# Kernel optimization log

Hardware: AMD Instinct MI355X
Metric: run time of the kernel (lower is better)

Reference implementation:

```python
import jax, jax.numpy as jnp
import numpy as np

DIM = 5120
NUM_HEADS = 40
HEAD_DIM = DIM // NUM_HEADS
EPS = 1e-6


def rms_norm(x, g):
    # RMSNorm over last dim in fp32 for stability
    xf = x.astype(jnp.float32)
    inv = jax.lax.rsqrt(jnp.mean(xf * xf, axis=-1, keepdims=True) + EPS)
    return (xf * inv).astype(x.dtype) * g


def setup_inputs() -> dict:
    key = jax.random.key(0)
    ks = jax.random.split(key, 12)
    B, S, L = 1, 4096, 512
    inp = {
        "hidden_cond": jax.random.normal(ks[0], (B, S, DIM), jnp.float32),
        "hidden_uncond": jax.random.normal(ks[1], (B, S, DIM), jnp.float32),
        "context_cond": jax.random.normal(ks[2], (B, L, DIM), jnp.float32),
        "context_uncond": jax.random.normal(ks[3], (B, L, DIM), jnp.float32),
        # parameters (torch nn.Linear: y = x @ W.T + b)
        "Wq": jax.random.normal(ks[4], (DIM, DIM), jnp.float32) * (DIM ** -0.5),
        "bq": jnp.zeros((DIM,), jnp.float32),
        "Wkv": jax.random.normal(ks[5], (2 * DIM, DIM), jnp.float32) * (DIM ** -0.5),
        "bkv": jnp.zeros((2 * DIM,), jnp.float32),
        "gq": jnp.ones((DIM,), jnp.float32),
        "gk": jnp.ones((DIM,), jnp.float32),
        "Wo": jax.random.normal(ks[6], (DIM, DIM), jnp.float32) * (DIM ** -0.5),
        "bo": jnp.zeros((DIM,), jnp.float32),
    }
    return inp


def reference(hidden_cond, hidden_uncond, context_cond, context_uncond,
              Wq, bq, Wkv, bkv, gq, gk, Wo, bo):
    H, Dh = NUM_HEADS, HEAD_DIM
    scale = Dh ** -0.5

    hidden = jnp.concatenate([hidden_cond, hidden_uncond], axis=0)   # [2B, S, D]
    context = jnp.concatenate([context_cond, context_uncond], axis=0)  # [2B, L, D]
    CB, S, D = hidden.shape
    L = context.shape[1]

    q = hidden @ Wq.T + bq                    # [2B, S, D]
    q = rms_norm(q, gq)
    q = q.reshape(CB, S, H, Dh).transpose(0, 2, 1, 3)  # [2B, H, S, Dh]

    kv = context @ Wkv.T + bkv                # [2B, L, 2D]
    kv = kv.reshape(CB, L, 2, H, Dh).transpose(2, 0, 3, 1, 4)  # [2,2B,H,L,Dh]
    k, v = kv[0], kv[1]

    k_flat = k.transpose(0, 2, 1, 3).reshape(CB, L, D)
    k_flat = rms_norm(k_flat, gk)
    k = k_flat.reshape(CB, L, H, Dh).transpose(0, 2, 1, 3)  # [2B, H, L, Dh]

    attn = jnp.einsum('bhsd,bhld->bhsl', q, k) * scale
    attn = jax.nn.softmax(attn.astype(jnp.float32), axis=-1).astype(q.dtype)
    out = jnp.einsum('bhsl,bhld->bhsd', attn, v)            # [2B, H, S, Dh]
    out = out.transpose(0, 2, 1, 3).reshape(CB, S, D)
    out = out @ Wo.T + bo

    out_cond, out_uncond = jnp.split(out, 2, axis=0)
    return (out_cond, out_uncond)
```

## Files before the change

### kernel.cpp

```cpp
#include <hip/hip_runtime.h>
#include <hip/hip_bf16.h>
#include <cstdint>
#include <cstddef>

#define DIM 5120
#define NH 40
#define HD 128
#define S_LEN 4096
#define L_LEN 512
#define CBATCH 2
#define MQ (CBATCH*S_LEN)
#define ML (CBATCH*L_LEN)

typedef unsigned short ushort_t;
typedef __bf16 bf16x8 __attribute__((ext_vector_type(8)));
typedef float f32x4 __attribute__((ext_vector_type(4)));
typedef float f32x16 __attribute__((ext_vector_type(16)));

__device__ __forceinline__ ushort_t f2bf(float f) {
  union { float f; unsigned u; } c; c.f = f;
  unsigned r = c.u + 0x7fffu + ((c.u >> 16) & 1u);
  return (ushort_t)(r >> 16);
}

__device__ __forceinline__ void load_lds16(const void* g, void* l) {
  __builtin_amdgcn_global_load_lds(
      (const __attribute__((address_space(1))) void*)g,
      (__attribute__((address_space(3))) void*)l, 16, 0, 0);
}

__global__ __launch_bounds__(256) void cvt_f32_bf16(const float* __restrict__ in,
                                                    ushort_t* __restrict__ out, int n4) {
  int i = blockIdx.x * 256 + threadIdx.x;
  if (i >= n4) return;
  float4 v = *(const float4*)(in + 4ull * (size_t)i);
  ushort4 o;
  o.x = f2bf(v.x); o.y = f2bf(v.y); o.z = f2bf(v.z); o.w = f2bf(v.w);
  *(ushort4*)(out + 4ull * (size_t)i) = o;
}

template <int OUT_F32>
__global__ __launch_bounds__(512, 2) void gemm_bt8(const ushort_t* __restrict__ A,
                                                   const ushort_t* __restrict__ W,
                                                   const float* __restrict__ bias,
                                                   void* __restrict__ Cout,
                                                   int M, int N, int K) {
  __shared__ ushort_t lds[73728];
  char* ldsc = (char*)lds;
  const int tid = threadIdx.x;
  const int lane = tid & 63, w = tid >> 6;
  const int g = lane >> 4, c = lane & 15;
  const int wm = w >> 2, wn = w & 3;
  const int ntn = N >> 8;
  const int nwg = gridDim.x;
  int bid = blockIdx.x;
  bid = (bid & 7) * (nwg >> 3) + (bid >> 3);
  const int tm = bid / ntn, tn = bid % ntn;
  const size_t m0 = (size_t)tm * 256, n0 = (size_t)tn * 256;
  const ushort_t* Ab = A + m0 * (size_t)K;
  const ushort_t* Bb = W + n0 * (size_t)K;
  const int NT = K >> 6;

  const int srow = tid >> 2;
  const int sgq  = (tid & 3) ^ (((tid >> 5) & 1) << 1);
  const size_t rb0 = (size_t)srow * K + (size_t)sgq * 8;
  const size_t rb1 = rb0 + (size_t)128 * K;
  const int d0 = tid * 16;

  int offA[8], offB[4];
#pragma unroll
  for (int m = 0; m < 8; ++m) {
    int row = wm * 128 + m * 16 + c;
    offA[m] = row * 64 + ((g * 16) ^ ((row & 8) << 2));
  }
#pragma unroll
  for (int n = 0; n < 4; ++n) {
    int row = wn * 64 + n * 16 + c;
    offB[n] = row * 64 + ((g * 16) ^ ((row & 8) << 2));
  }

  auto STAGE = [&](int tIdx, int j, int dOff) {
    const size_t kof = (size_t)tIdx * 64 + (size_t)((j >> 1) << 5);
    const ushort_t* gsrc = ((j & 1) ? Ab : Bb) + kof;
    char* db = ldsc + dOff;
    load_lds16(gsrc + rb0, db + d0);
    load_lds16(gsrc + rb1, db + 8192 + d0);
  };
  auto nx = [](int x) { return (x + 16384 == 147456) ? 0 : x + 16384; };

  f32x4 acc[8][4] = {};

#pragma unroll
  for (int h = 0; h < 8; ++h) STAGE(h >> 2, h & 3, h * 16384);
  asm volatile("s_waitcnt vmcnt(8)" ::: "memory");
  __builtin_amdgcn_s_barrier();

  int rd = 0;
  int sOff = 131072;
  for (int t = 0; t < NT; ++t) {
    const int r0 = rd, r1 = nx(r0), r2 = nx(r1), r3 = nx(r2);
    bf16x8 a[4], a2[4], b[4];
#pragma unroll
    for (int m = 0; m < 4; ++m) a[m] = *(const bf16x8*)(ldsc + r1 + offA[m]);
#pragma unroll
    for (int n = 0; n < 4; ++n) b[n] = *(const bf16x8*)(ldsc + r0 + offB[n]);
    if (t < NT - 2) { STAGE(t + 2, 0, sOff); sOff = nx(sOff); }
    __builtin_amdgcn_s_barrier();
    asm volatile("s_waitcnt lgkmcnt(0)" ::: "memory");
    __builtin_amdgcn_sched_barrier(0);
    __builtin_amdgcn_s_setprio(1);
#pragma unroll
    for (int m = 0; m < 4; ++m)
#pragma unroll
      for (int n = 0; n < 4; ++n)
        acc[m][n] = __builtin_amdgcn_mfma_f32_16x16x32_bf16(a[m], b[n], acc[m][n], 0, 0, 0);
    __builtin_amdgcn_s_setprio(0);
    __builtin_amdgcn_s_barrier();
#pragma unroll
    for (int m = 0; m < 4; ++m) a2[m] = *(const bf16x8*)(ldsc + r1 + offA[4 + m]);
    if (t < NT - 2) { STAGE(t + 2, 1, sOff); sOff = nx(sOff); }
    __builtin_amdgcn_s_barrier();
    asm volatile("s_waitcnt lgkmcnt(0)" ::: "memory");
    __builtin_amdgcn_sched_barrier(0);
    __builtin_amdgcn_s_setprio(1);
#pragma unroll
    for (int m = 0; m < 4; ++m)
#pragma unroll
      for (int n = 0; n < 4; ++n)
        acc[4 + m][n] = __builtin_amdgcn_mfma_f32_16x16x32_bf16(a2[m], b[n], acc[4 + m][n], 0, 0, 0);
    __builtin_amdgcn_s_setprio(0);
    __builtin_amdgcn_s_barrier();
#pragma unroll
    for (int m = 0; m < 4; ++m) a[m] = *(const bf16x8*)(ldsc + r3 + offA[m]);
#pragma unroll
    for (int n = 0; n < 4; ++n) b[n] = *(const bf16x8*)(ldsc + r2 + offB[n]);
    if (t < NT - 2) { STAGE(t + 2, 2, sOff); sOff = nx(sOff); }
    __builtin_amdgcn_s_barrier();
    asm volatile("s_waitcnt lgkmcnt(0)" ::: "memory");
    __builtin_amdgcn_sched_barrier(0);
    __builtin_amdgcn_s_setprio(1);
#pragma unroll
    for (int m = 0; m < 4; ++m)
#pragma unroll
      for (int n = 0; n < 4; ++n)
        acc[m][n] = __builtin_amdgcn_mfma_f32_16x16x32_bf16(a[m], b[n], acc[m][n], 0, 0, 0);
    __builtin_amdgcn_s_setprio(0);
    __builtin_amdgcn_s_barrier();
#pragma unroll
    for (int m = 0; m < 4; ++m) a2[m] = *(const bf16x8*)(ldsc + r3 + offA[4 + m]);
    if (t < NT - 2) { STAGE(t + 2, 3, sOff); sOff = nx(sOff); }
    __builtin_amdgcn_s_barrier();
    asm volatile("s_waitcnt lgkmcnt(0)" ::: "memory");
    __builtin_amdgcn_sched_barrier(0);
    __builtin_amdgcn_s_setprio(1);
#pragma unroll
    for (int m = 0; m < 4; ++m)
#pragma unroll
      for (int n = 0; n < 4; ++n)
        acc[4 + m][n] = __builtin_amdgcn_mfma_f32_16x16x32_bf16(a2[m], b[n], acc[4 + m][n], 0, 0, 0);
    __builtin_amdgcn_s_setprio(0);
    if (t < NT - 2)       asm volatile("s_waitcnt vmcnt(6)" ::: "memory");
    else if (t == NT - 2) asm volatile("s_waitcnt vmcnt(0)" ::: "memory");
    __builtin_amdgcn_s_barrier();
    rd = nx(r3);
  }

#pragma unroll
  for (int m = 0; m < 8; ++m) {
#pragma unroll
    for (int n = 0; n < 4; ++n) {
      size_t gm = m0 + wm * 128 + m * 16 + g * 4;
      size_t gn = n0 + wn * 64 + n * 16 + c;
      float bn = bias[gn];
#pragma unroll
      for (int r = 0; r < 4; ++r) {
        float v = acc[m][n][r] + bn;
        if (OUT_F32) ((float*)Cout)[(gm + r) * (size_t)N + gn] = v;
        else         ((ushort_t*)Cout)[(gm + r) * (size_t)N + gn] = f2bf(v);
      }
    }
  }
  (void)M;
}

template <int OUT_F32>
__global__ __launch_bounds__(256) void gemm_bt(const ushort_t* __restrict__ A,
                                               const ushort_t* __restrict__ W,
                                               const float* __restrict__ bias,
                                               void* __restrict__ Cout,
                                               int M, int N, int K) {
  __shared__ ushort_t sA[128 * 32];
  __shared__ ushort_t sB[128 * 32];
  const int tid = threadIdx.x;
  const int w = tid >> 6, lane = tid & 63;
  const int g = lane >> 4, c = lane & 15;
  const int ntn = N >> 7;
  const int nwg = gridDim.x;
  int bid = blockIdx.x;
  bid = (bid & 7) * (nwg >> 3) + (bid >> 3);
  const int tm = bid / ntn, tn = bid % ntn;
  const size_t m0 = (size_t)tm * 128, n0 = (size_t)tn * 128;
  const int wr = (w >> 1) * 64, wc = (w & 1) * 64;

  f32x4 acc[4][4] = {};

  const ushort_t* Abase = A + m0 * (size_t)K;
  const ushort_t* Bbase = W + n0 * (size_t)K;

  for (int k0 = 0; k0 < K; k0 += 32) {
    __syncthreads();
#pragma unroll
    for (int i = 0; i < 2; ++i) {
      int gid = i * 256 + tid;
      int row = gid >> 2, colE = (gid & 3) << 3;
      load_lds16(Abase + (size_t)row * K + k0 + colE, sA + i * 2048 + w * 512);
      load_lds16(Bbase + (size_t)row * K + k0 + colE, sB + i * 2048 + w * 512);
    }
    __syncthreads();
    bf16x8 a[4], b[4];
#pragma unroll
    for (int m = 0; m < 4; ++m)
      a[m] = *(const bf16x8*)(sA + (wr + m * 16 + c) * 32 + g * 8);
#pragma unroll
    for (int n = 0; n < 4; ++n)
      b[n] = *(const bf16x8*)(sB + (wc + n * 16 + c) * 32 + g * 8);
#pragma unroll
    for (int m = 0; m < 4; ++m)
#pragma unroll
      for (int n = 0; n < 4; ++n)
        acc[m][n] = __builtin_amdgcn_mfma_f32_16x16x32_bf16(a[m], b[n], acc[m][n], 0, 0, 0);
  }

#pragma unroll
  for (int m = 0; m < 4; ++m) {
#pragma unroll
    for (int n = 0; n < 4; ++n) {
      size_t gm = m0 + wr + m * 16 + g * 4;
      size_t gn = n0 + wc + n * 16 + c;
      float bn = bias[gn];
#pragma unroll
      for (int r = 0; r < 4; ++r) {
        float v = acc[m][n][r] + bn;
        if (OUT_F32) ((float*)Cout)[(gm + r) * (size_t)N + gn] = v;
        else         ((ushort_t*)Cout)[(gm + r) * (size_t)N + gn] = f2bf(v);
      }
    }
  }
}

__global__ __launch_bounds__(256) void rmsnorm_rows(ushort_t* __restrict__ x,
                                                    const float* __restrict__ gw,
                                                    int ncols, int stride, float oscale) {
  const int row = blockIdx.x;
  ushort_t* p = x + (size_t)row * stride;
  const int tid = threadIdx.x;
  const int nch = ncols >> 3;
  float ss = 0.f;
  for (int ci = tid; ci < nch; ci += 256) {
    bf16x8 v = *(const bf16x8*)(p + ci * 8);
#pragma unroll
    for (int j = 0; j < 8; ++j) { float f = (float)v[j]; ss += f * f; }
  }
#pragma unroll
  for (int off = 1; off < 64; off <<= 1) ss += __shfl_xor(ss, off);
  __shared__ float sred[4];
  if ((tid & 63) == 0) sred[tid >> 6] = ss;
  __syncthreads();
  float tot = sred[0] + sred[1] + sred[2] + sred[3];
  float inv = rsqrtf(tot / (float)ncols + 1e-6f) * oscale;
  for (int ci = tid; ci < nch; ci += 256) {
    bf16x8 v = *(const bf16x8*)(p + ci * 8);
    bf16x8 ov;
#pragma unroll
    for (int j = 0; j < 8; ++j) {
      float f = (float)v[j];
      ushort_t ob = f2bf(f * inv * gw[ci * 8 + j]);
      ov[j] = *(__bf16*)&ob;
    }
    *(bf16x8*)(p + ci * 8) = ov;
  }
}

__global__ __launch_bounds__(256) void transpose_v(const ushort_t* __restrict__ kv,
                                                   ushort_t* __restrict__ vt) {
  const int bh = blockIdx.y, b = bh / NH, h = bh % NH;
  const int l0 = blockIdx.x * 32;
  const ushort_t* src = kv + (size_t)b * L_LEN * (2 * DIM) + DIM + (size_t)h * HD;
  ushort_t* dst = vt + (size_t)bh * HD * L_LEN;
  __shared__ ushort_t tile[32][HD + 16];
  const int tid = threadIdx.x;
#pragma unroll
  for (int i = 0; i < 2; ++i) {
    int gid = i * 256 + tid;
    int r = gid >> 4, ce = (gid & 15) << 3;
    *(bf16x8*)(&tile[r][ce]) = *(const bf16x8*)(src + (size_t)(l0 + r) * (2 * DIM) + ce);
  }
  __syncthreads();
#pragma unroll
  for (int i = 0; i < 2; ++i) {
    int gid = i * 256 + tid;
    int d = gid >> 2, le = (gid & 3) << 3;
    bf16x8 v;
#pragma unroll
    for (int j = 0; j < 8; ++j) v[j] = *(__bf16*)&tile[le + j][d];
    *(bf16x8*)(dst + (size_t)d * L_LEN + l0 + le) = v;
  }
}

__global__ __launch_bounds__(256) void attn_fwd(const ushort_t* __restrict__ q,
                                                const ushort_t* __restrict__ kv,
                                                const ushort_t* __restrict__ vt,
                                                ushort_t* __restrict__ out) {
  const int bh = blockIdx.y, b = bh / NH, h = bh % NH;
  const int tid = threadIdx.x, w = tid >> 6, lane = tid & 63;
  const int lq = lane & 31, hi = lane >> 5;
  const int qr0 = blockIdx.x * 128 + w * 32;

  __shared__ ushort_t sK[2][4096];
  __shared__ ushort_t sV[2][4096];

  const int skl = tid >> 3, skc = tid & 7;
  const ushort_t* kgsrc = kv + ((size_t)b * L_LEN + skl) * (2 * DIM)
                             + (size_t)h * HD + skc * 16;
  ushort_t* kd0 = &sK[0][(skc * 2) * 256 + skl * 8];
  ushort_t* kd1 = &sK[0][(skc * 2 + 1) * 256 + skl * 8];
  const int svd = tid >> 1, svh = tid & 1;
  const ushort_t* vgsrc = vt + (size_t)bh * HD * L_LEN + (size_t)svd * L_LEN + svh * 16;
  ushort_t* vd0 = &sV[0][(svh * 2) * 1024 + svd * 8];
  ushort_t* vd1 = &sV[0][(svh * 2 + 1) * 1024 + svd * 8];

  const ushort_t* qrow = q + ((size_t)b * S_LEN + qr0 + lq) * DIM + (size_t)h * HD + hi * 8;
  bf16x8 qf[8];
#pragma unroll
  for (int ks = 0; ks < 8; ++ks) qf[ks] = *(const bf16x8*)(qrow + ks * 16);

  f32x16 o[4];
#pragma unroll
  for (int ch = 0; ch < 4; ++ch) o[ch] = 0.f;
  float m = -1e30f, lsum = 0.f;

  {
    uint4 ka = *(const uint4*)kgsrc;
    uint4 kb = *(const uint4*)(kgsrc + 8);
    uint4 va = *(const uint4*)vgsrc;
    uint4 vb = *(const uint4*)(vgsrc + 8);
    *(uint4*)kd0 = ka; *(uint4*)kd1 = kb;
    *(uint4*)vd0 = va; *(uint4*)vd1 = vb;
  }
  __syncthreads();

  const int NT = L_LEN / 32;
  int buf = 0;
  for (int t = 0; t < NT; ++t) {
    uint4 ka, kb, va, vb;
    if (t + 1 < NT) {
      const ushort_t* kg = kgsrc + (size_t)(t + 1) * 32 * (2 * DIM);
      const ushort_t* vg = vgsrc + (t + 1) * 32;
      ka = *(const uint4*)kg; kb = *(const uint4*)(kg + 8);
      va = *(const uint4*)vg; vb = *(const uint4*)(vg + 8);
    }

    const ushort_t* kbuf = sK[buf];
    const ushort_t* vbuf = sV[buf];

    f32x16 sv = 0.f;
#pragma unroll
    for (int ks = 0; ks < 8; ++ks) {
      bf16x8 kf = *(const bf16x8*)(kbuf + (ks * 2 + hi) * 256 + lq * 8);
      sv = __builtin_amdgcn_mfma_f32_32x32x16_bf16(kf, qf[ks], sv, 0, 0, 0);
    }
    float pm = fmaxf(fmaxf(fmaxf(sv[0], sv[1]), fmaxf(sv[2], sv[3])),
                     fmaxf(fmaxf(sv[4], sv[5]), fmaxf(sv[6], sv[7])));
    pm = fmaxf(pm, fmaxf(fmaxf(fmaxf(sv[8], sv[9]), fmaxf(sv[10], sv[11])),
                         fmaxf(fmaxf(sv[12], sv[13]), fmaxf(sv[14], sv[15]))));
    pm = fmaxf(pm, __shfl_xor(pm, 32));
    if (__ballot(pm > m + 8.0f)) {
      float mn = fmaxf(m, pm);
      float al = __builtin_amdgcn_exp2f(m - mn);
      lsum *= al;
      m = mn;
#pragma unroll
      for (int r = 0; r < 16; ++r) {
        float ar = __shfl(al, (r & 3) + 8 * (r >> 2) + 4 * hi);
        o[0][r] *= ar; o[1][r] *= ar; o[2][r] *= ar; o[3][r] *= ar;
      }
    }
    float p[16]; float ls = 0.f;
#pragma unroll
    for (int r = 0; r < 16; ++r) { p[r] = __builtin_amdgcn_exp2f(sv[r] - m); ls += p[r]; }
    ls += __shfl_xor(ls, 32);
    lsum += ls;
    bf16x8 pa[2];
#pragma unroll
    for (int ks = 0; ks < 2; ++ks) {
      unsigned w0 = (unsigned)f2bf(p[8 * ks + 0]) | ((unsigned)f2bf(p[8 * ks + 1]) << 16);
      unsigned w1 = (unsigned)f2bf(p[8 * ks + 2]) | ((unsigned)f2bf(p[8 * ks + 3]) << 16);
      unsigned w2 = (unsigned)f2bf(p[8 * ks + 4]) | ((unsigned)f2bf(p[8 * ks + 5]) << 16);
      unsigned w3 = (unsigned)f2bf(p[8 * ks + 6]) | ((unsigned)f2bf(p[8 * ks + 7]) << 16);
      unsigned e0 = __shfl_xor((int)w0, 32), e1 = __shfl_xor((int)w1, 32);
      unsigned e2 = __shfl_xor((int)w2, 32), e3 = __shfl_xor((int)w3, 32);
      unsigned d0 = hi ? e2 : w0, d1 = hi ? e3 : w1;
      unsigned d2 = hi ? w2 : e0, d3 = hi ? w3 : e1;
      unsigned tmp[4] = {d0, d1, d2, d3};
      pa[ks] = *(const bf16x8*)tmp;
    }
#pragma unroll
    for (int ch = 0; ch < 4; ++ch) {
#pragma unroll
      for (int ks = 0; ks < 2; ++ks) {
        bf16x8 vf = *(const bf16x8*)(vbuf + (ks * 2 + hi) * 1024 + (ch * 32 + lq) * 8);
        o[ch] = __builtin_amdgcn_mfma_f32_32x32x16_bf16(pa[ks], vf, o[ch], 0, 0, 0);
      }
    }

    if (t + 1 < NT) {
      const int nb = buf ^ 1;
      *(uint4*)(kd0 + nb * 4096) = ka; *(uint4*)(kd1 + nb * 4096) = kb;
      *(uint4*)(vd0 + nb * 4096) = va; *(uint4*)(vd1 + nb * 4096) = vb;
    }
    __syncthreads();
    buf ^= 1;
  }

  float inv[16];
#pragma unroll
  for (int r = 0; r < 16; ++r) {
    float lr = __shfl(lsum, (r & 3) + 8 * (r >> 2) + 4 * hi);
    inv[r] = 1.0f / lr;
  }
  ushort_t* ob = out + ((size_t)b * S_LEN + qr0) * DIM + (size_t)h * HD;
#pragma unroll
  for (int ch = 0; ch < 4; ++ch)
#pragma unroll
    for (int r = 0; r < 16; ++r) {
      int row = (r & 3) + 8 * (r >> 2) + 4 * hi;
      ob[(size_t)row * DIM + ch * 32 + lq] = f2bf(o[ch][r] * inv[r]);
    }
}

extern "C" void kernel_launch(void* const* d_in, const int* in_sizes, int n_in,
                              void* d_out, int out_size, void* d_ws, size_t ws_size,
                              hipStream_t stream) {
  (void)in_sizes; (void)n_in; (void)out_size; (void)ws_size;
  const float* hidden_c = (const float*)d_in[0];
  const float* hidden_u = (const float*)d_in[1];
  const float* ctx_c    = (const float*)d_in[2];
  const float* ctx_u    = (const float*)d_in[3];
  const float* Wq  = (const float*)d_in[4];
  const float* bq  = (const float*)d_in[5];
  const float* Wkv = (const float*)d_in[6];
  const float* bkv = (const float*)d_in[7];
  const float* gq  = (const float*)d_in[8];
  const float* gk  = (const float*)d_in[9];
  const float* Wo  = (const float*)d_in[10];
  const float* bo  = (const float*)d_in[11];

  char* ws = (char*)d_ws;
  size_t off = 0;
  auto alloc = [&](size_t bytes) {
    char* p = ws + off; off += (bytes + 255) & ~(size_t)255; return p;
  };
  ushort_t* hbf  = (ushort_t*)alloc((size_t)MQ * DIM * 2);
  ushort_t* cbf  = (ushort_t*)alloc((size_t)ML * DIM * 2);
  ushort_t* wqb  = (ushort_t*)alloc((size_t)DIM * DIM * 2);
  ushort_t* wkvb = (ushort_t*)alloc((size_t)2 * DIM * DIM * 2);
  ushort_t* kvb  = (ushort_t*)alloc((size_t)ML * 2 * DIM * 2);
  ushort_t* vtb  = (ushort_t*)alloc((size_t)CBATCH * NH * HD * L_LEN * 2);
  ushort_t* qb   = (ushort_t*)d_out;

  auto cvt = [&](const float* in, ushort_t* o, size_t n) {
    int n4 = (int)(n >> 2);
    cvt_f32_bf16<<<dim3((n4 + 255) / 256), dim3(256), 0, stream>>>(in, o, n4);
  };
  cvt(hidden_c, hbf, (size_t)S_LEN * DIM);
  cvt(hidden_u, hbf + (size_t)S_LEN * DIM, (size_t)S_LEN * DIM);
  cvt(ctx_c, cbf, (size_t)L_LEN * DIM);
  cvt(ctx_u, cbf + (size_t)L_LEN * DIM, (size_t)L_LEN * DIM);
  cvt(Wq, wqb, (size_t)DIM * DIM);
  cvt(Wkv, wkvb, (size_t)2 * DIM * DIM);

  gemm_bt8<0><<<dim3((MQ / 256) * (DIM / 256)), dim3(512), 0, stream>>>(
      hbf, wqb, bq, (void*)qb, MQ, DIM, DIM);
  gemm_bt<0><<<dim3((ML / 128) * ((2 * DIM) / 128)), dim3(256), 0, stream>>>(
      cbf, wkvb, bkv, (void*)kvb, ML, 2 * DIM, DIM);
  cvt(Wo, wqb, (size_t)DIM * DIM);

  const float qscale = 0.08838834764831845f * 1.4426950408889634f;
  rmsnorm_rows<<<dim3(MQ), dim3(256), 0, stream>>>(qb, gq, DIM, DIM, qscale);
  rmsnorm_rows<<<dim3(ML), dim3(256), 0, stream>>>(kvb, gk, DIM, 2 * DIM, 1.0f);
  transpose_v<<<dim3(L_LEN / 32, CBATCH * NH), dim3(256), 0, stream>>>(kvb, vtb);

  attn_fwd<<<dim3(S_LEN / 128, CBATCH * NH), dim3(256), 0, stream>>>(qb, kvb, vtb, hbf);

  gemm_bt8<1><<<dim3((MQ / 256) * (DIM / 256)), dim3(512), 0, stream>>>(
      hbf, wqb, bo, d_out, MQ, DIM, DIM);
}
```

Baseline: 1.432 ms.

## Fuse Q and KV projection GEMMs into one launch using the 256x256 core

Extracts the 256x256 MFMA GEMM body into a shared device function and launches the Q projection and KV projection as one 800-block grid, with blocks 0-639 doing Q and the rest doing KV. The KV projection moves from the simpler 128x128 tile kernel to the larger pipelined tile. K is made a compile-time constant. The intent is to remove the weak KV GEMM and fill the tail of the Q GEMM wave with KV work, at the cost of hard-coded grid sizes and block swizzling across the mixed grid.

```diff
diff --git a/kernel.cpp b/kernel.cpp
--- a/kernel.cpp
+++ b/kernel.cpp
@@ -40,26 +40,18 @@
 }
 
 template <int OUT_F32>
-__global__ __launch_bounds__(512, 2) void gemm_bt8(const ushort_t* __restrict__ A,
-                                                   const ushort_t* __restrict__ W,
-                                                   const float* __restrict__ bias,
-                                                   void* __restrict__ Cout,
-                                                   int M, int N, int K) {
-  __shared__ ushort_t lds[73728];
-  char* ldsc = (char*)lds;
+__device__ __forceinline__ void gemm_core(const ushort_t* __restrict__ Ab,
+                                          const ushort_t* __restrict__ Bb,
+                                          const float* __restrict__ bias,
+                                          void* __restrict__ Cout,
+                                          int N, size_t m0, size_t n0,
+                                          char* ldsc) {
   const int tid = threadIdx.x;
   const int lane = tid & 63, w = tid >> 6;
   const int g = lane >> 4, c = lane & 15;
   const int wm = w >> 2, wn = w & 3;
-  const int ntn = N >> 8;
-  const int nwg = gridDim.x;
-  int bid = blockIdx.x;
-  bid = (bid & 7) * (nwg >> 3) + (bid >> 3);
-  const int tm = bid / ntn, tn = bid % ntn;
-  const size_t m0 = (size_t)tm * 256, n0 = (size_t)tn * 256;
-  const ushort_t* Ab = A + m0 * (size_t)K;
-  const ushort_t* Bb = W + n0 * (size_t)K;
-  const int NT = K >> 6;
+  constexpr int K = DIM;
+  constexpr int NT = K >> 6;
 
   const int srow = tid >> 2;
   const int sgq  = (tid & 3) ^ (((tid >> 5) & 1) << 1);
@@ -180,72 +172,41 @@
       }
     }
   }
-  (void)M;
-}
-
-template <int OUT_F32>
-__global__ __launch_bounds__(256) void gemm_bt(const ushort_t* __restrict__ A,
-                                               const ushort_t* __restrict__ W,
-                                               const float* __restrict__ bias,
-                                               void* __restrict__ Cout,
-                                               int M, int N, int K) {
-  __shared__ ushort_t sA[128 * 32];
-  __shared__ ushort_t sB[128 * 32];
-  const int tid = threadIdx.x;
-  const int w = tid >> 6, lane = tid & 63;
-  const int g = lane >> 4, c = lane & 15;
-  const int ntn = N >> 7;
-  const int nwg = gridDim.x;
+}
+
+__global__ __launch_bounds__(512, 2) void gemm_fused_qkv(
+    const ushort_t* __restrict__ hbf, const ushort_t* __restrict__ wq,
+    const ushort_t* __restrict__ cbf, const ushort_t* __restrict__ wkv,
+    const float* __restrict__ bq, const float* __restrict__ bkv,
+    ushort_t* __restrict__ qb, ushort_t* __restrict__ kvb) {
+  __shared__ ushort_t lds[73728];
+  char* ldsc = (char*)lds;
+  const int nwg = 800;
   int bid = blockIdx.x;
   bid = (bid & 7) * (nwg >> 3) + (bid >> 3);
-  const int tm = bid / ntn, tn = bid % ntn;
-  const size_t m0 = (size_t)tm * 128, n0 = (size_t)tn * 128;
-  const int wr = (w >> 1) * 64, wc = (w & 1) * 64;
-
-  f32x4 acc[4][4] = {};
-
-  const ushort_t* Abase = A + m0 * (size_t)K;
-  const ushort_t* Bbase = W + n0 * (size_t)K;
-
-  for (int k0 = 0; k0 < K; k0 += 32) {
-    __syncthreads();
-#pragma unroll
-    for (int i = 0; i < 2; ++i) {
-      int gid = i * 256 + tid;
-      int row = gid >> 2, colE = (gid & 3) << 3;
-      load_lds16(Abase + (size_t)row * K + k0 + colE, sA + i * 2048 + w * 512);
-      load_lds16(Bbase + (size_t)row * K + k0 + colE, sB + i * 2048 + w * 512);
-    }
-    __syncthreads();
-    bf16x8 a[4], b[4];
-#pragma unroll
-    for (int m = 0; m < 4; ++m)
-      a[m] = *(const bf16x8*)(sA + (wr + m * 16 + c) * 32 + g * 8);
-#pragma unroll
-    for (int n = 0; n < 4; ++n)
-      b[n] = *(const bf16x8*)(sB + (wc + n * 16 + c) * 32 + g * 8);
-#pragma unroll
-    for (int m = 0; m < 4; ++m)
-#pragma unroll
-      for (int n = 0; n < 4; ++n)
-        acc[m][n] = __builtin_amdgcn_mfma_f32_16x16x32_bf16(a[m], b[n], acc[m][n], 0, 0, 0);
-  }
-
-#pragma unroll
-  for (int m = 0; m < 4; ++m) {
-#pragma unroll
-    for (int n = 0; n < 4; ++n) {
-      size_t gm = m0 + wr + m * 16 + g * 4;
-      size_t gn = n0 + wc + n * 16 + c;
-      float bn = bias[gn];
-#pragma unroll
-      for (int r = 0; r < 4; ++r) {
-        float v = acc[m][n][r] + bn;
-        if (OUT_F32) ((float*)Cout)[(gm + r) * (size_t)N + gn] = v;
-        else         ((ushort_t*)Cout)[(gm + r) * (size_t)N + gn] = f2bf(v);
-      }
-    }
-  }
+  if (bid < 640) {
+    const int tm = bid / 20, tn = bid % 20;
+    const size_t m0 = (size_t)tm * 256, n0 = (size_t)tn * 256;
+    gemm_core<0>(hbf + m0 * DIM, wq + n0 * DIM, bq, qb, DIM, m0, n0, ldsc);
+  } else {
+    const int e = bid - 640;
+    const int tm = e / 40, tn = e % 40;
+    const size_t m0 = (size_t)tm * 256, n0 = (size_t)tn * 256;
+    gemm_core<0>(cbf + m0 * DIM, wkv + n0 * DIM, bkv, kvb, 2 * DIM, m0, n0, ldsc);
+  }
+}
+
+__global__ __launch_bounds__(512, 2) void gemm_out(
+    const ushort_t* __restrict__ A, const ushort_t* __restrict__ W,
+    const float* __restrict__ bias, float* __restrict__ C) {
+  __shared__ ushort_t lds[73728];
+  char* ldsc = (char*)lds;
+  const int nwg = 640;
+  int bid = blockIdx.x;
+  bid = (bid & 7) * (nwg >> 3) + (bid >> 3);
+  const int tm = bid / 20, tn = bid % 20;
+  const size_t m0 = (size_t)tm * 256, n0 = (size_t)tn * 256;
+  gemm_core<1>(A + m0 * DIM, W + n0 * DIM, bias, C, DIM, m0, n0, ldsc);
 }
 
 __global__ __launch_bounds__(256) void rmsnorm_rows(ushort_t* __restrict__ x,
@@ -479,10 +440,8 @@
   cvt(Wq, wqb, (size_t)DIM * DIM);
   cvt(Wkv, wkvb, (size_t)2 * DIM * DIM);
 
-  gemm_bt8<0><<<dim3((MQ / 256) * (DIM / 256)), dim3(512), 0, stream>>>(
-      hbf, wqb, bq, (void*)qb, MQ, DIM, DIM);
-  gemm_bt<0><<<dim3((ML / 128) * ((2 * DIM) / 128)), dim3(256), 0, stream>>>(
-      cbf, wkvb, bkv, (void*)kvb, ML, 2 * DIM, DIM);
+  gemm_fused_qkv<<<dim3(800), dim3(512), 0, stream>>>(
+      hbf, wqb, cbf, wkvb, bq, bkv, qb, kvb);
   cvt(Wo, wqb, (size_t)DIM * DIM);
 
   const float qscale = 0.08838834764831845f * 1.4426950408889634f;
@@ -492,6 +451,5 @@
 
   attn_fwd<<<dim3(S_LEN / 128, CBATCH * NH), dim3(256), 0, stream>>>(qb, kvb, vtb, hbf);
 
-  gemm_bt8<1><<<dim3((MQ / 256) * (DIM / 256)), dim3(512), 0, stream>>>(
-      hbf, wqb, bo, d_out, MQ, DIM, DIM);
-}
+  gemm_out<<<dim3(640), dim3(512), 0, stream>>>(hbf, wqb, bo, (float*)d_out);
+}
```

After: 1.371 ms. 1.04x faster.

## Fuse Q and KV projections into one launch and split GEMMs to reduce tail waves

Applied to the files above, without the earlier changes.

The 256x256-tile GEMM body becomes a device function specialised for K=DIM. The Q projection and most of the KV projection now run in a single 768-block launch, and the last 2048 KV columns go to a small 128x128-tile kernel. The output projection is split the same way: 512 big-tile blocks cover 4096 columns and a 128x128-tile kernel covers the remaining 1024. The aim is to cut wave-quantisation tails of the 640-block GEMMs at two blocks per CU, and to run the KV GEMM on the efficient big-tile path, at the cost of an extra launch whose small tiles reuse data less.

```diff
diff --git a/kernel.cpp b/kernel.cpp
--- a/kernel.cpp
+++ b/kernel.cpp
@@ -40,26 +40,18 @@
 }
 
 template <int OUT_F32>
-__global__ __launch_bounds__(512, 2) void gemm_bt8(const ushort_t* __restrict__ A,
-                                                   const ushort_t* __restrict__ W,
-                                                   const float* __restrict__ bias,
-                                                   void* __restrict__ Cout,
-                                                   int M, int N, int K) {
-  __shared__ ushort_t lds[73728];
-  char* ldsc = (char*)lds;
+__device__ __forceinline__ void gemm_core(const ushort_t* __restrict__ Ab,
+                                          const ushort_t* __restrict__ Bb,
+                                          const float* __restrict__ bias,
+                                          void* __restrict__ Cout,
+                                          int N, size_t m0, size_t n0,
+                                          char* ldsc) {
   const int tid = threadIdx.x;
   const int lane = tid & 63, w = tid >> 6;
   const int g = lane >> 4, c = lane & 15;
   const int wm = w >> 2, wn = w & 3;
-  const int ntn = N >> 8;
-  const int nwg = gridDim.x;
-  int bid = blockIdx.x;
-  bid = (bid & 7) * (nwg >> 3) + (bid >> 3);
-  const int tm = bid / ntn, tn = bid % ntn;
-  const size_t m0 = (size_t)tm * 256, n0 = (size_t)tn * 256;
-  const ushort_t* Ab = A + m0 * (size_t)K;
-  const ushort_t* Bb = W + n0 * (size_t)K;
-  const int NT = K >> 6;
+  constexpr int K = DIM;
+  constexpr int NT = K >> 6;
 
   const int srow = tid >> 2;
   const int sgq  = (tid & 3) ^ (((tid >> 5) & 1) << 1);
@@ -180,27 +172,59 @@
       }
     }
   }
-  (void)M;
+}
+
+__global__ __launch_bounds__(512, 2) void gemm_fused_qkv(
+    const ushort_t* __restrict__ hbf, const ushort_t* __restrict__ wq,
+    const ushort_t* __restrict__ cbf, const ushort_t* __restrict__ wkv,
+    const float* __restrict__ bq, const float* __restrict__ bkv,
+    ushort_t* __restrict__ qb, ushort_t* __restrict__ kvb) {
+  __shared__ ushort_t lds[73728];
+  char* ldsc = (char*)lds;
+  int bid = blockIdx.x;
+  bid = (bid & 7) * 96 + (bid >> 3);
+  if (bid < 640) {
+    const int tm = bid / 20, tn = bid % 20;
+    const size_t m0 = (size_t)tm * 256, n0 = (size_t)tn * 256;
+    gemm_core<0>(hbf + m0 * DIM, wq + n0 * DIM, bq, qb, DIM, m0, n0, ldsc);
+  } else {
+    const int e = bid - 640;
+    const int tm = e >> 5, tn = e & 31;
+    const size_t m0 = (size_t)tm * 256, n0 = (size_t)tn * 256;
+    gemm_core<0>(cbf + m0 * DIM, wkv + n0 * DIM, bkv, kvb, 2 * DIM, m0, n0, ldsc);
+  }
+}
+
+__global__ __launch_bounds__(512, 2) void gemm_out_main(
+    const ushort_t* __restrict__ A, const ushort_t* __restrict__ W,
+    const float* __restrict__ bias, float* __restrict__ C) {
+  __shared__ ushort_t lds[73728];
+  char* ldsc = (char*)lds;
+  int bid = blockIdx.x;
+  bid = (bid & 7) * 64 + (bid >> 3);
+  const int tm = bid / 16, tn = bid % 16;
+  const size_t m0 = (size_t)tm * 256, n0 = (size_t)tn * 256;
+  gemm_core<1>(A + m0 * DIM, W + n0 * DIM, bias, C, DIM, m0, n0, ldsc);
 }
 
 template <int OUT_F32>
-__global__ __launch_bounds__(256) void gemm_bt(const ushort_t* __restrict__ A,
-                                               const ushort_t* __restrict__ W,
-                                               const float* __restrict__ bias,
-                                               void* __restrict__ Cout,
-                                               int M, int N, int K) {
+__global__ __launch_bounds__(256) void gemm_bt_region(const ushort_t* __restrict__ A,
+                                                      const ushort_t* __restrict__ W,
+                                                      const float* __restrict__ bias,
+                                                      void* __restrict__ Cout,
+                                                      int strideN, int ntn) {
   __shared__ ushort_t sA[128 * 32];
   __shared__ ushort_t sB[128 * 32];
   const int tid = threadIdx.x;
   const int w = tid >> 6, lane = tid & 63;
   const int g = lane >> 4, c = lane & 15;
-  const int ntn = N >> 7;
   const int nwg = gridDim.x;
   int bid = blockIdx.x;
   bid = (bid & 7) * (nwg >> 3) + (bid >> 3);
   const int tm = bid / ntn, tn = bid % ntn;
   const size_t m0 = (size_t)tm * 128, n0 = (size_t)tn * 128;
   const int wr = (w >> 1) * 64, wc = (w & 1) * 64;
+  constexpr int K = DIM;
 
   f32x4 acc[4][4] = {};
 
@@ -241,8 +265,8 @@
 #pragma unroll
       for (int r = 0; r < 4; ++r) {
         float v = acc[m][n][r] + bn;
-        if (OUT_F32) ((float*)Cout)[(gm + r) * (size_t)N + gn] = v;
-        else         ((ushort_t*)Cout)[(gm + r) * (size_t)N + gn] = f2bf(v);
+        if (OUT_F32) ((float*)Cout)[(gm + r) * (size_t)strideN + gn] = v;
+        else         ((ushort_t*)Cout)[(gm + r) * (size_t)strideN + gn] = f2bf(v);
       }
     }
   }
@@ -479,10 +503,10 @@
   cvt(Wq, wqb, (size_t)DIM * DIM);
   cvt(Wkv, wkvb, (size_t)2 * DIM * DIM);
 
-  gemm_bt8<0><<<dim3((MQ / 256) * (DIM / 256)), dim3(512), 0, stream>>>(
-      hbf, wqb, bq, (void*)qb, MQ, DIM, DIM);
-  gemm_bt<0><<<dim3((ML / 128) * ((2 * DIM) / 128)), dim3(256), 0, stream>>>(
-      cbf, wkvb, bkv, (void*)kvb, ML, 2 * DIM, DIM);
+  gemm_fused_qkv<<<dim3(768), dim3(512), 0, stream>>>(
+      hbf, wqb, cbf, wkvb, bq, bkv, qb, kvb);
+  gemm_bt_region<0><<<dim3(128), dim3(256), 0, stream>>>(
+      cbf, wkvb + (size_t)8192 * DIM, bkv + 8192, kvb + 8192, 2 * DIM, 16);
   cvt(Wo, wqb, (size_t)DIM * DIM);
 
   const float qscale = 0.08838834764831845f * 1.4426950408889634f;
@@ -492,6 +516,7 @@
 
   attn_fwd<<<dim3(S_LEN / 128, CBATCH * NH), dim3(256), 0, stream>>>(qb, kvb, vtb, hbf);
 
-  gemm_bt8<1><<<dim3((MQ / 256) * (DIM / 256)), dim3(512), 0, stream>>>(
-      hbf, wqb, bo, d_out, MQ, DIM, DIM);
-}
+  gemm_out_main<<<dim3(512), dim3(512), 0, stream>>>(hbf, wqb, bo, (float*)d_out);
+  gemm_bt_region<1><<<dim3(512), dim3(256), 0, stream>>>(
+      hbf, wqb + (size_t)4096 * DIM, bo + 4096, (float*)d_out + 4096, DIM, 8);
+}
```

After: 1.392 ms. -2.8%, faster.
